# Optimization experiments

Hardware: AMD Instinct MI355X
Metric: run time of the kernel (lower is better)

## Reference

```python
import jax, jax.numpy as jnp
import numpy as np

B, S, IN_DIM, OUT_DIM = 16, 1024, 1024, 1024
NEG_SLOPE = 0.01  # torch F.leaky_relu default


def setup_inputs() -> dict:
    key = jax.random.key(0)
    ks = jax.random.split(key, 10)
    sc_in = 1.0 / np.sqrt(IN_DIM)
    sc_out = 1.0 / np.sqrt(OUT_DIM)
    return {
        "xs": jax.random.normal(ks[0], (B, S, IN_DIM), dtype=jnp.float32),
        "mask": jax.random.randint(ks[1], (B, S), 0, 2, dtype=jnp.int32),
        "Wk": jax.random.uniform(ks[2], (OUT_DIM, IN_DIM), jnp.float32, -sc_in, sc_in),
        "bk": jax.random.uniform(ks[3], (OUT_DIM,), jnp.float32, -sc_in, sc_in),
        "Wq": jax.random.uniform(ks[4], (OUT_DIM, IN_DIM), jnp.float32, -sc_in, sc_in),
        "bq": jax.random.uniform(ks[5], (OUT_DIM,), jnp.float32, -sc_in, sc_in),
        "Wv": jax.random.uniform(ks[6], (OUT_DIM, IN_DIM), jnp.float32, -sc_in, sc_in),
        "bv": jax.random.uniform(ks[7], (OUT_DIM,), jnp.float32, -sc_in, sc_in),
        "Wlin": jax.random.uniform(ks[8], (OUT_DIM, OUT_DIM), jnp.float32, -sc_out, sc_out),
        "blin": jax.random.uniform(ks[9], (OUT_DIM,), jnp.float32, -sc_out, sc_out),
    }


def reference(xs, mask, Wk, bk, Wq, bq, Wv, bv, Wlin, blin):
    # projections: torch Linear is x @ W.T + b
    K = jnp.einsum('bsi,oi->bso', xs, Wk) + bk  # [B,S,D]
    Q = jnp.einsum('bsi,oi->bso', xs, Wq) + bq  # [B,S,D]
    V = jnp.einsum('bsi,oi->bso', xs, Wv) + bv  # [B,S,D]
    # qk[b,s,e] = sum_d K[b,s,d] * Q[b,e,d]
    qk = jnp.einsum('bsd,bed->bse', K, Q) / xs.shape[-1]
    # mask.repeat(1,S).view(B,S,S) => element [b,i,j] = mask[b,j] (column/key mask)
    qk = jnp.where(mask[:, None, :].astype(bool), qk, -jnp.inf)
    a = jax.nn.softmax(qk, axis=-1)  # [B,S,S]
    # faithful to einsum('bij,bik->bik'): sum a over last axis, scale V elementwise
    attn = jnp.sum(a, axis=-1, keepdims=True) * V  # [B,S,D]
    out = jnp.einsum('bsd,od->bso', attn, Wlin) + blin
    return jnp.where(out >= 0, out, NEG_SLOPE * out)
```

## Files before the change

### kernel.cpp

```cpp
#include <hip/hip_runtime.h>
#include <hip/hip_bf16.h>
#include <stdint.h>


#define M_TOT 16384
#define KDIM  1024
#define NDIM  1024
#define NKT   16

typedef __attribute__((ext_vector_type(8))) short bf16x8;
typedef __attribute__((ext_vector_type(4))) float f32x4;
typedef __attribute__((ext_vector_type(4))) unsigned short u16x4;
typedef __attribute__((ext_vector_type(8))) unsigned short u16x8;

static __device__ __forceinline__ unsigned short f2bf(float f) {
    union { float f; unsigned int u; } v; v.f = f;
    unsigned int u = v.u;
    return (unsigned short)((u + 0x7fffu + ((u >> 16) & 1u)) >> 16);
}

static __device__ __forceinline__ u16x8 pack8(float4 a, float4 b) {
    u16x8 p = { f2bf(a.x), f2bf(a.y), f2bf(a.z), f2bf(a.w),
                f2bf(b.x), f2bf(b.y), f2bf(b.z), f2bf(b.w) };
    return p;
}

static __device__ __forceinline__ void gload16(const void* g, void* l) {
    __builtin_amdgcn_global_load_lds(
        (__attribute__((address_space(1))) void*)(g),
        (__attribute__((address_space(3))) void*)(l), 16, 0, 0);
}

static __device__ __forceinline__ int swz128(int p) {
    return p ^ (((p >> 7) & 7) << 4);
}

__global__ __launch_bounds__(256) void prep0_kernel(
    const float* __restrict__ Wv, const float* __restrict__ Wlin,
    const float* __restrict__ bv, const float* __restrict__ blin,
    unsigned short* __restrict__ Wvt, unsigned short* __restrict__ Wlb,
    float* __restrict__ bcomb) {
    __shared__ float Tl[64 * 65];
    const int bid = blockIdx.x;
    const int t = threadIdx.x;

    if (bid < 256) {
        const int dt = bid >> 4;
        const int it = bid & 15;
        const int r = t >> 2;
        const int c0 = (t & 3) * 16;
        #pragma unroll
        for (int u = 0; u < 4; ++u) {
            float4 v = *(const float4*)&Wv[((size_t)(dt * 64 + r)) * NDIM + it * 64 + c0 + 4 * u];
            Tl[r * 65 + c0 + 4 * u + 0] = v.x;
            Tl[r * 65 + c0 + 4 * u + 1] = v.y;
            Tl[r * 65 + c0 + 4 * u + 2] = v.z;
            Tl[r * 65 + c0 + 4 * u + 3] = v.w;
        }
        __syncthreads();
        const int i = t >> 2;
        const int dq = (t & 3) * 16;
        float v[16];
        #pragma unroll
        for (int u = 0; u < 16; ++u) v[u] = Tl[(dq + u) * 65 + i];
        u16x8 p0 = { f2bf(v[0]), f2bf(v[1]), f2bf(v[2]), f2bf(v[3]),
                     f2bf(v[4]), f2bf(v[5]), f2bf(v[6]), f2bf(v[7]) };
        u16x8 p1 = { f2bf(v[8]), f2bf(v[9]), f2bf(v[10]), f2bf(v[11]),
                     f2bf(v[12]), f2bf(v[13]), f2bf(v[14]), f2bf(v[15]) };
        unsigned short* dst = &Wvt[((size_t)(it * 64 + i)) * KDIM + dt * 64 + dq];
        *(u16x8*)dst = p0;
        *(u16x8*)(dst + 8) = p1;
    } else if (bid < 512) {
        const size_t idx = (((size_t)(bid - 256)) * 256 + t) * 16;
        float4 a = *(const float4*)&Wlin[idx];
        float4 b = *(const float4*)&Wlin[idx + 4];
        float4 c = *(const float4*)&Wlin[idx + 8];
        float4 d = *(const float4*)&Wlin[idx + 12];
        *(u16x8*)&Wlb[idx] = pack8(a, b);
        *(u16x8*)&Wlb[idx + 8] = pack8(c, d);
    } else {
        const int wave = t >> 6, lane = t & 63;
        const int o = (bid - 512) * 4 + wave;
        float s = 0.f;
        for (int d = lane; d < KDIM; d += 64) s += Wlin[o * KDIM + d] * bv[d];
        #pragma unroll
        for (int off = 32; off > 0; off >>= 1) s += __shfl_down(s, off, 64);
        if (lane == 0) bcomb[o] = s + blin[o];
    }
}

__global__ __launch_bounds__(256) void wcomb_kernel(
    const unsigned short* __restrict__ Wlb, const unsigned short* __restrict__ Wvt,
    unsigned short* __restrict__ Wc) {
    __shared__ unsigned short As[64 * 32];
    __shared__ unsigned short Bs[64 * 32];
    const int t = threadIdx.x;
    const int ot = blockIdx.x >> 4;
    const int it = blockIdx.x & 15;
    const int w = t >> 6, l = t & 63;
    const int wr = (w >> 1) * 32, wc = (w & 1) * 32;
    const int lr = l & 15, lk = l >> 4;

    f32x4 acc[2][2] = {};

    const unsigned short* gA = &Wlb[((size_t)(ot * 64 + (t >> 2))) * KDIM + (t & 3) * 8];
    const unsigned short* gB = &Wvt[((size_t)(it * 64 + (t >> 2))) * KDIM + (t & 3) * 8];
    unsigned short* lA = &As[w * 512];
    unsigned short* lB = &Bs[w * 512];

    for (int kt = 0; kt < KDIM / 32; ++kt) {
        gload16(gA + kt * 32, lA);
        gload16(gB + kt * 32, lB);
        __syncthreads();
        bf16x8 af[2], bfr[2];
        #pragma unroll
        for (int fi = 0; fi < 2; ++fi)
            af[fi] = *(bf16x8*)&As[(wr + fi * 16 + lr) * 32 + lk * 8];
        #pragma unroll
        for (int fj = 0; fj < 2; ++fj)
            bfr[fj] = *(bf16x8*)&Bs[(wc + fj * 16 + lr) * 32 + lk * 8];
        #pragma unroll
        for (int fi = 0; fi < 2; ++fi)
            #pragma unroll
            for (int fj = 0; fj < 2; ++fj)
                acc[fi][fj] = __builtin_amdgcn_mfma_f32_16x16x32_bf16(
                    af[fi], bfr[fj], acc[fi][fj], 0, 0, 0);
        __syncthreads();
    }
    #pragma unroll
    for (int fi = 0; fi < 2; ++fi)
        #pragma unroll
        for (int fj = 0; fj < 2; ++fj)
            #pragma unroll
            for (int r = 0; r < 4; ++r) {
                const int o = ot * 64 + wr + fi * 16 + lk * 4 + r;
                const int i = it * 64 + wc + fj * 16 + lr;
                Wc[(size_t)o * KDIM + i] = f2bf(acc[fi][fj][r]);
            }
}

__global__ __launch_bounds__(512, 2) void main_fused(
    const float* __restrict__ xs, const unsigned short* __restrict__ Wc,
    const float* __restrict__ bcomb, float* __restrict__ out) {
    extern __shared__ char lds[];
    const int tid = threadIdx.x;
    const int w = tid >> 6, l = tid & 63;
    const int wm = w >> 2, wn = w & 3;
    const int lr = l & 15, lk = l >> 4;

    const int swzb = ((blockIdx.x & 7) << 5) + (blockIdx.x >> 3);
    const int mt = swzb >> 2, nt = swzb & 3;

    int aoff[8], boff[4];
    #pragma unroll
    for (int fi = 0; fi < 8; ++fi)
        aoff[fi] = swz128((wm * 128 + fi * 16 + lr) * 128 + lk * 16);
    #pragma unroll
    for (int fj = 0; fj < 4; ++fj)
        boff[fj] = 32768 + swz128((wn * 64 + fj * 16 + lr) * 128 + lk * 16);

    const float* gA[4];
    int awr[4];
    #pragma unroll
    for (int j = 0; j < 4; ++j) {
        const int row = j * 64 + (tid >> 3);
        gA[j] = xs + ((size_t)(mt * 256 + row)) * KDIM + (tid & 7) * 8;
        awr[j] = swz128(row * 128 + (tid & 7) * 16);
    }
    const char* gB[4];
    #pragma unroll
    for (int j = 0; j < 4; ++j) {
        const int q = j * 8192 + w * 1024 + l * 16;
        const int p = swz128(q);
        gB[j] = (const char*)Wc + ((size_t)(nt * 256 + (p >> 7))) * 2048 + (p & 127);
    }
    const int bofs[4] = { 32768 + w * 1024, 32768 + 8192 + w * 1024,
                          32768 + 16384 + w * 1024, 32768 + 24576 + w * 1024 };

    f32x4 acc[8][4] = {};
    float4 avA[8];

#define STAGE_A(TT)                                                            \
    _Pragma("unroll")                                                          \
    for (int j = 0; j < 4; ++j) {                                              \
        avA[2 * j]     = *(const float4*)(gA[j] + (TT) * 64);                  \
        avA[2 * j + 1] = *(const float4*)(gA[j] + (TT) * 64 + 4);              \
    }

    STAGE_A(0);
    #pragma unroll
    for (int j = 0; j < 4; ++j)
        gload16(gB[j], lds + bofs[j]);
    *(u16x8*)(lds + awr[0]) = pack8(avA[0], avA[1]);
    *(u16x8*)(lds + awr[1]) = pack8(avA[2], avA[3]);
    *(u16x8*)(lds + awr[2]) = pack8(avA[4], avA[5]);
    *(u16x8*)(lds + awr[3]) = pack8(avA[6], avA[7]);
    asm volatile("s_waitcnt vmcnt(0)" ::: "memory");
    asm volatile("s_waitcnt lgkmcnt(0)" ::: "memory");
    __builtin_amdgcn_s_barrier();

#define MFMA16(ACCI, AF, BF)                                                   \
    _Pragma("unroll")                                                          \
    for (int fi = 0; fi < 4; ++fi)                                             \
        _Pragma("unroll")                                                      \
        for (int fj = 0; fj < 4; ++fj)                                         \
            acc[(ACCI) + fi][fj] = __builtin_amdgcn_mfma_f32_16x16x32_bf16(    \
                (AF)[fi], (BF)[fj], acc[(ACCI) + fi][fj], 0, 0, 0)

#define PH_SYNC()                                                              \
    __builtin_amdgcn_s_barrier();                                              \
    asm volatile("s_waitcnt lgkmcnt(0)" ::: "memory");                         \
    __builtin_amdgcn_sched_barrier(0)

#define ITER(T, SEN, WN)                                                       \
    do {                                                                       \
        const char* cbuf = lds + (((T) & 1) << 16);                            \
        char* nbuf = lds + ((((T) & 1) ^ 1) << 16);                            \
        if (SEN) {                                                             \
            STAGE_A((T) + 1);                                                  \
            gload16(gB[0] + ((size_t)(T) + 1) * 128, nbuf + bofs[0]);          \
            gload16(gB[1] + ((size_t)(T) + 1) * 128, nbuf + bofs[1]);          \
            gload16(gB[2] + ((size_t)(T) + 1) * 128, nbuf + bofs[2]);          \
            gload16(gB[3] + ((size_t)(T) + 1) * 128, nbuf + bofs[3]);          \
        }                                                                      \
        asm volatile("s_waitcnt vmcnt(" #WN ")" ::: "memory");                 \
        __builtin_amdgcn_s_barrier();                                          \
                                               \
        bf16x8 b0[4], a0[4];                                                   \
        _Pragma("unroll")                                                      \
        for (int fj = 0; fj < 4; ++fj)                                         \
            b0[fj] = *(const bf16x8*)(cbuf + boff[fj]);                        \
        _Pragma("unroll")                                                      \
        for (int fi = 0; fi < 4; ++fi)                                         \
            a0[fi] = *(const bf16x8*)(cbuf + aoff[fi]);                        \
        PH_SYNC();                                                             \
        __builtin_amdgcn_s_setprio(1);                                         \
        MFMA16(0, a0, b0);                                                     \
        __builtin_amdgcn_s_setprio(0);                                         \
        __builtin_amdgcn_s_barrier();                                          \
                                                       \
        bf16x8 a1[4];                                                          \
        _Pragma("unroll")                                                      \
        for (int fi = 0; fi < 4; ++fi)                                         \
            a1[fi] = *(const bf16x8*)(cbuf + aoff[4 + fi]);                    \
        PH_SYNC();                                                             \
        __builtin_amdgcn_s_setprio(1);                                         \
        MFMA16(4, a1, b0);                                                     \
        __builtin_amdgcn_s_setprio(0);                                         \
        __builtin_amdgcn_s_barrier();                                          \
                    \
        bf16x8 b1[4], a2[4];                                                   \
        _Pragma("unroll")                                                      \
        for (int fj = 0; fj < 4; ++fj)                                         \
            b1[fj] = *(const bf16x8*)(cbuf + (boff[fj] ^ 64));                 \
        _Pragma("unroll")                                                      \
        for (int fi = 0; fi < 4; ++fi)                                         \
            a2[fi] = *(const bf16x8*)(cbuf + (aoff[fi] ^ 64));                 \
        PH_SYNC();                                                             \
        __builtin_amdgcn_s_setprio(1);                                         \
        MFMA16(0, a2, b1);                                                     \
        __builtin_amdgcn_s_setprio(0);                                         \
        if (SEN) {                                                             \
            *(u16x8*)(nbuf + awr[0]) = pack8(avA[0], avA[1]);                  \
            *(u16x8*)(nbuf + awr[1]) = pack8(avA[2], avA[3]);                  \
        }                                                                      \
        __builtin_amdgcn_s_barrier();                                          \
                            \
        bf16x8 a3[4];                                                          \
        _Pragma("unroll")                                                      \
        for (int fi = 0; fi < 4; ++fi)                                         \
            a3[fi] = *(const bf16x8*)(cbuf + (aoff[4 + fi] ^ 64));             \
        PH_SYNC();                                                             \
        __builtin_amdgcn_s_setprio(1);                                         \
        MFMA16(4, a3, b1);                                                     \
        __builtin_amdgcn_s_setprio(0);                                         \
        if (SEN) {                                                             \
            *(u16x8*)(nbuf + awr[2]) = pack8(avA[4], avA[5]);                  \
            *(u16x8*)(nbuf + awr[3]) = pack8(avA[6], avA[7]);                  \
        }                                                                      \
    } while (0)

    for (int t = 0; t < NKT - 1; ++t) {
        ITER(t, 1, 12);
    }
    ITER(15, 0, 0);
#undef ITER
#undef PH_SYNC
#undef MFMA16
#undef STAGE_A

    #pragma unroll
    for (int fi = 0; fi < 8; ++fi)
        #pragma unroll
        for (int fj = 0; fj < 4; ++fj) {
            const int col = nt * 256 + wn * 64 + fj * 16 + lr;
            const float b = bcomb[col];
            #pragma unroll
            for (int r = 0; r < 4; ++r) {
                const int row = mt * 256 + wm * 128 + fi * 16 + lk * 4 + r;
                float v = acc[fi][fj][r] + b;
                out[(size_t)row * NDIM + col] = v >= 0.f ? v : 0.01f * v;
            }
        }
}

__global__ __launch_bounds__(256) void main_gemm_f32(
    const float* __restrict__ X, const unsigned short* __restrict__ Wc,
    const float* __restrict__ bcomb, float* __restrict__ out) {
    __shared__ unsigned short As[128 * 32];
    __shared__ unsigned short Bs[128 * 32];
    const int t = threadIdx.x;
    const int nt = blockIdx.x & 7;
    const int mt = blockIdx.x >> 3;
    const int w = t >> 6, l = t & 63;
    const int wr = (w >> 1) * 64, wcc = (w & 1) * 64;
    const int lr = l & 15, lk = l >> 4;

    f32x4 acc[4][4] = {};

    const int arow = t >> 3;
    const int akq = t & 7;
    const int brow = t >> 2;
    const int bc4 = t & 3;

    for (int kt = 0; kt < KDIM / 32; ++kt) {
        float4 av[4];
        #pragma unroll
        for (int j = 0; j < 4; ++j) {
            const int row = j * 32 + arow;
            av[j] = *(const float4*)&X[(mt * 128 + row) * KDIM + kt * 32 + akq * 4];
        }
        __syncthreads();
        #pragma unroll
        for (int j = 0; j < 4; ++j) {
            const int row = j * 32 + arow;
            u16x4 p = { f2bf(av[j].x), f2bf(av[j].y), f2bf(av[j].z), f2bf(av[j].w) };
            *(u16x4*)&As[row * 32 + akq * 4] = p;
        }
        #pragma unroll
        for (int j = 0; j < 2; ++j) {
            const int row = j * 64 + brow;
            const unsigned short* g = &Wc[(nt * 128 + row) * KDIM + kt * 32 + bc4 * 8];
            unsigned short* ldst = &Bs[(j * 256 + w * 64) * 8];
            gload16(g, ldst);
        }
        __syncthreads();
        bf16x8 af[4], bfr[4];
        #pragma unroll
        for (int fi = 0; fi < 4; ++fi)
            af[fi] = *(bf16x8*)&As[(wr + fi * 16 + lr) * 32 + lk * 8];
        #pragma unroll
        for (int fj = 0; fj < 4; ++fj)
            bfr[fj] = *(bf16x8*)&Bs[(wcc + fj * 16 + lr) * 32 + lk * 8];
        #pragma unroll
        for (int fi = 0; fi < 4; ++fi)
            #pragma unroll
            for (int fj = 0; fj < 4; ++fj)
                acc[fi][fj] = __builtin_amdgcn_mfma_f32_16x16x32_bf16(
                    af[fi], bfr[fj], acc[fi][fj], 0, 0, 0);
    }

    #pragma unroll
    for (int fi = 0; fi < 4; ++fi)
        #pragma unroll
        for (int fj = 0; fj < 4; ++fj) {
            const int col = nt * 128 + wcc + fj * 16 + lr;
            const float b = bcomb[col];
            #pragma unroll
            for (int r = 0; r < 4; ++r) {
                const int row = mt * 128 + wr + fi * 16 + lk * 4 + r;
                float v = acc[fi][fj][r] + b;
                out[row * NDIM + col] = v >= 0.f ? v : 0.01f * v;
            }
        }
}

extern "C" void kernel_launch(void* const* d_in, const int* in_sizes, int n_in,
                              void* d_out, int out_size, void* d_ws, size_t ws_size,
                              hipStream_t stream) {
    const float* xs   = (const float*)d_in[0];
    const float* Wv   = (const float*)d_in[6];
    const float* bv   = (const float*)d_in[7];
    const float* Wlin = (const float*)d_in[8];
    const float* blin = (const float*)d_in[9];

    unsigned short* Wc = (unsigned short*)d_ws;
    float* bcomb = (float*)((char*)d_ws + 2097152);
    float* out = (float*)d_out;

    unsigned short* Wvt = (unsigned short*)d_out;
    unsigned short* Wlb = (unsigned short*)((char*)d_out + 2097152);

    const size_t NEED = 2101248;
    hipLaunchKernelGGL(prep0_kernel, dim3(768), dim3(256), 0, stream,
                       Wv, Wlin, bv, blin, Wvt, Wlb, bcomb);
    hipLaunchKernelGGL(wcomb_kernel, dim3(256), dim3(256), 0, stream,
                       Wlb, Wvt, Wc);
    if (ws_size >= NEED) {
        (void)hipFuncSetAttribute((const void*)main_fused,
                                  hipFuncAttributeMaxDynamicSharedMemorySize,
                                  131072);
        hipLaunchKernelGGL(main_fused, dim3(256), dim3(512), 131072, stream,
                           xs, Wc, bcomb, out);
    } else {
        hipLaunchKernelGGL(main_gemm_f32, dim3((M_TOT / 128) * (NDIM / 128)),
                           dim3(256), 0, stream, xs, Wc, bcomb, out);
    }
}
```

Baseline: 79.13 us.

## Switch fused GEMM to 4-buffer ring with 32-wide K tiles and prefetch depth two

Halves the K tile from 64 to 32 elements and uses a four-slot LDS ring instead of double buffering, so global loads for A and B are issued two iterations ahead. The LDS swizzle is changed to fit the 64-byte row layout, and each iteration is reduced from four sync phases to two. The goal is to hide global-load latency better and cut barrier and waitcnt overhead per MFMA block. In exchange there are twice as many iterations, each with less work between barriers, and the new swizzle may cause more LDS bank conflicts.

```diff
diff --git a/kernel.cpp b/kernel.cpp
--- a/kernel.cpp
+++ b/kernel.cpp
@@ -6,7 +6,7 @@
 #define M_TOT 16384
 #define KDIM  1024
 #define NDIM  1024
-#define NKT   16
+#define NKT   32
 
 typedef __attribute__((ext_vector_type(8))) short bf16x8;
 typedef __attribute__((ext_vector_type(4))) float f32x4;
@@ -31,8 +31,8 @@
         (__attribute__((address_space(3))) void*)(l), 16, 0, 0);
 }
 
-static __device__ __forceinline__ int swz128(int p) {
-    return p ^ (((p >> 7) & 7) << 4);
+static __device__ __forceinline__ int swz(int p) {
+    return p ^ (((p >> 9) & 1) << 5) ^ (((p >> 8) & 1) << 4);
 }
 
 __global__ __launch_bounds__(256) void prep0_kernel(
@@ -154,48 +154,55 @@
     int aoff[8], boff[4];
     #pragma unroll
     for (int fi = 0; fi < 8; ++fi)
-        aoff[fi] = swz128((wm * 128 + fi * 16 + lr) * 128 + lk * 16);
+        aoff[fi] = swz((wm * 128 + fi * 16 + lr) * 64 + lk * 16);
     #pragma unroll
     for (int fj = 0; fj < 4; ++fj)
-        boff[fj] = 32768 + swz128((wn * 64 + fj * 16 + lr) * 128 + lk * 16);
-
-    const float* gA[4];
-    int awr[4];
-    #pragma unroll
-    for (int j = 0; j < 4; ++j) {
-        const int row = j * 64 + (tid >> 3);
-        gA[j] = xs + ((size_t)(mt * 256 + row)) * KDIM + (tid & 7) * 8;
-        awr[j] = swz128(row * 128 + (tid & 7) * 16);
-    }
-    const char* gB[4];
-    #pragma unroll
-    for (int j = 0; j < 4; ++j) {
-        const int q = j * 8192 + w * 1024 + l * 16;
-        const int p = swz128(q);
-        gB[j] = (const char*)Wc + ((size_t)(nt * 256 + (p >> 7))) * 2048 + (p & 127);
-    }
-    const int bofs[4] = { 32768 + w * 1024, 32768 + 8192 + w * 1024,
-                          32768 + 16384 + w * 1024, 32768 + 24576 + w * 1024 };
+        boff[fj] = 16384 + swz((wn * 64 + fj * 16 + lr) * 64 + lk * 16);
+
+    const float* gAq[2];
+    const char* gBq[2];
+    #pragma unroll
+    for (int c = 0; c < 2; ++c) {
+        const int q = c * 8192 + tid * 16;
+        const int p = swz(q);
+        const int row = p >> 6;
+        const int colb = p & 63;
+        gAq[c] = xs + ((size_t)(mt * 256 + row)) * KDIM + (colb >> 1);
+        gBq[c] = (const char*)Wc + ((size_t)(nt * 256 + row)) * 2048 + colb;
+    }
+    const int ldsA0 = tid * 16;
+    const int ldsA1 = 8192 + tid * 16;
+    const int ldsBw = 16384 + w * 1024;
 
     f32x4 acc[8][4] = {};
-    float4 avA[8];
-
-#define STAGE_A(TT)                                                            \
-    _Pragma("unroll")                                                          \
-    for (int j = 0; j < 4; ++j) {                                              \
-        avA[2 * j]     = *(const float4*)(gA[j] + (TT) * 64);                  \
-        avA[2 * j + 1] = *(const float4*)(gA[j] + (TT) * 64 + 4);              \
-    }
-
-    STAGE_A(0);
-    #pragma unroll
-    for (int j = 0; j < 4; ++j)
-        gload16(gB[j], lds + bofs[j]);
-    *(u16x8*)(lds + awr[0]) = pack8(avA[0], avA[1]);
-    *(u16x8*)(lds + awr[1]) = pack8(avA[2], avA[3]);
-    *(u16x8*)(lds + awr[2]) = pack8(avA[4], avA[5]);
-    *(u16x8*)(lds + awr[3]) = pack8(avA[6], avA[7]);
-    asm volatile("s_waitcnt vmcnt(0)" ::: "memory");
+    float4 avA[4];
+
+#define LOAD_A(TT)                                                             \
+    do {                                                                       \
+        avA[0] = *(const float4*)(gAq[0] + (TT) * 32);                         \
+        avA[1] = *(const float4*)(gAq[0] + (TT) * 32 + 4);                     \
+        avA[2] = *(const float4*)(gAq[1] + (TT) * 32);                         \
+        avA[3] = *(const float4*)(gAq[1] + (TT) * 32 + 4);                     \
+    } while (0)
+
+#define CVT_A(BUF)                                                             \
+    do {                                                                       \
+        *(u16x8*)((BUF) + ldsA0) = pack8(avA[0], avA[1]);                      \
+        *(u16x8*)((BUF) + ldsA1) = pack8(avA[2], avA[3]);                      \
+    } while (0)
+
+#define GLOAD_B(TT, BUF)                                                       \
+    do {                                                                       \
+        gload16(gBq[0] + (size_t)(TT) * 64, (BUF) + ldsBw);                    \
+        gload16(gBq[1] + (size_t)(TT) * 64, (BUF) + 8192 + ldsBw);             \
+    } while (0)
+
+    LOAD_A(0);
+    GLOAD_B(0, lds);
+    CVT_A(lds);
+    LOAD_A(1);
+    GLOAD_B(1, lds + 32768);
+    CVT_A(lds + 32768);
     asm volatile("s_waitcnt lgkmcnt(0)" ::: "memory");
     __builtin_amdgcn_s_barrier();
 
@@ -207,87 +214,52 @@
             acc[(ACCI) + fi][fj] = __builtin_amdgcn_mfma_f32_16x16x32_bf16(    \
                 (AF)[fi], (BF)[fj], acc[(ACCI) + fi][fj], 0, 0, 0)
 
-#define PH_SYNC()                                                              \
-    __builtin_amdgcn_s_barrier();                                              \
-    asm volatile("s_waitcnt lgkmcnt(0)" ::: "memory");                         \
-    __builtin_amdgcn_sched_barrier(0)
-
 #define ITER(T, SEN, WN)                                                       \
     do {                                                                       \
-        const char* cbuf = lds + (((T) & 1) << 16);                            \
-        char* nbuf = lds + ((((T) & 1) ^ 1) << 16);                            \
-        if (SEN) {                                                             \
-            STAGE_A((T) + 1);                                                  \
-            gload16(gB[0] + ((size_t)(T) + 1) * 128, nbuf + bofs[0]);          \
-            gload16(gB[1] + ((size_t)(T) + 1) * 128, nbuf + bofs[1]);          \
-            gload16(gB[2] + ((size_t)(T) + 1) * 128, nbuf + bofs[2]);          \
-            gload16(gB[3] + ((size_t)(T) + 1) * 128, nbuf + bofs[3]);          \
-        }                                                                      \
-        asm volatile("s_waitcnt vmcnt(" #WN ")" ::: "memory");                 \
-        __builtin_amdgcn_s_barrier();                                          \
-                                               \
-        bf16x8 b0[4], a0[4];                                                   \
+        const char* cbuf = lds + (size_t)((T) & 3) * 32768;                    \
+        char* stbuf = lds + (size_t)(((T) + 2) & 3) * 32768;                   \
+                  \
+        if (SEN) { LOAD_A((T) + 2); }                                          \
+        bf16x8 bfr[4], afr[4];                                                 \
         _Pragma("unroll")                                                      \
         for (int fj = 0; fj < 4; ++fj)                                         \
-            b0[fj] = *(const bf16x8*)(cbuf + boff[fj]);                        \
+            bfr[fj] = *(const bf16x8*)(cbuf + boff[fj]);                       \
         _Pragma("unroll")                                                      \
         for (int fi = 0; fi < 4; ++fi)                                         \
-            a0[fi] = *(const bf16x8*)(cbuf + aoff[fi]);                        \
-        PH_SYNC();                                                             \
+            afr[fi] = *(const bf16x8*)(cbuf + aoff[fi]);                       \
+        __builtin_amdgcn_s_barrier();                                          \
         __builtin_amdgcn_s_setprio(1);                                         \
-        MFMA16(0, a0, b0);                                                     \
+        MFMA16(0, afr, bfr);                                                   \
         __builtin_amdgcn_s_setprio(0);                                         \
         __builtin_amdgcn_s_barrier();                                          \
-                                                       \
-        bf16x8 a1[4];                                                          \
+                          \
+        if (SEN) { GLOAD_B((T) + 2, stbuf); }                                  \
+        bf16x8 af2[4];                                                         \
         _Pragma("unroll")                                                      \
         for (int fi = 0; fi < 4; ++fi)                                         \
-            a1[fi] = *(const bf16x8*)(cbuf + aoff[4 + fi]);                    \
-        PH_SYNC();                                                             \
+            af2[fi] = *(const bf16x8*)(cbuf + aoff[4 + fi]);                   \
+        __builtin_amdgcn_s_barrier();                                          \
         __builtin_amdgcn_s_setprio(1);                                         \
-        MFMA16(4, a1, b0);                                                     \
+        MFMA16(4, af2, bfr);                                                   \
         __builtin_amdgcn_s_setprio(0);                                         \
+            \
+        if (SEN) { CVT_A(stbuf); }                                             \
+                                                            \
+        asm volatile("s_waitcnt vmcnt(" #WN ")" ::: "memory");                 \
+        asm volatile("s_waitcnt lgkmcnt(0)" ::: "memory");                     \
         __builtin_amdgcn_s_barrier();                                          \
-                    \
-        bf16x8 b1[4], a2[4];                                                   \
-        _Pragma("unroll")                                                      \
-        for (int fj = 0; fj < 4; ++fj)                                         \
-            b1[fj] = *(const bf16x8*)(cbuf + (boff[fj] ^ 64));                 \
-        _Pragma("unroll")                                                      \
-        for (int fi = 0; fi < 4; ++fi)                                         \
-            a2[fi] = *(const bf16x8*)(cbuf + (aoff[fi] ^ 64));                 \
-        PH_SYNC();                                                             \
-        __builtin_amdgcn_s_setprio(1);                                         \
-        MFMA16(0, a2, b1);                                                     \
-        __builtin_amdgcn_s_setprio(0);                                         \
-        if (SEN) {                                                             \
-            *(u16x8*)(nbuf + awr[0]) = pack8(avA[0], avA[1]);                  \
-            *(u16x8*)(nbuf + awr[1]) = pack8(avA[2], avA[3]);                  \
-        }                                                                      \
-        __builtin_amdgcn_s_barrier();                                          \
-                            \
-        bf16x8 a3[4];                                                          \
-        _Pragma("unroll")                                                      \
-        for (int fi = 0; fi < 4; ++fi)                                         \
-            a3[fi] = *(const bf16x8*)(cbuf + (aoff[4 + fi] ^ 64));             \
-        PH_SYNC();                                                             \
-        __builtin_amdgcn_s_setprio(1);                                         \
-        MFMA16(4, a3, b1);                                                     \
-        __builtin_amdgcn_s_setprio(0);                                         \
-        if (SEN) {                                                             \
-            *(u16x8*)(nbuf + awr[2]) = pack8(avA[4], avA[5]);                  \
-            *(u16x8*)(nbuf + awr[3]) = pack8(avA[6], avA[7]);                  \
-        }                                                                      \
     } while (0)
 
-    for (int t = 0; t < NKT - 1; ++t) {
-        ITER(t, 1, 12);
-    }
-    ITER(15, 0, 0);
+    for (int t = 0; t < NKT - 2; ++t) {
+        ITER(t, 1, 2);
+    }
+    ITER(30, 0, 2);
+    ITER(31, 0, 0);
 #undef ITER
-#undef PH_SYNC
 #undef MFMA16
-#undef STAGE_A
+#undef GLOAD_B
+#undef CVT_A
+#undef LOAD_A
 
     #pragma unroll
     for (int fi = 0; fi < 8; ++fi)
```

Measured after the change: 82.21 us. +3.9%, slower.

## Pre-convert xs to bf16 in prep kernel and use direct-to-LDS loads for both operands

Applied to the files above, without the earlier changes.

Adds an xs-to-bf16 conversion pass to the weight-combining prep kernel, writing a bf16 copy of the activations into workspace. The main GEMM then loads both A and B tiles straight into LDS with async global loads, replacing the fp32 register staging, packing and LDS writes. B is prefetched two tiles ahead and A one tile ahead, with the waits and barriers rearranged to match. This removes conversion and LDS-store work from the GEMM's inner loop. In exchange, the xs array is read in fp32 once and written plus re-read in bf16, which adds extra memory traffic and a larger workspace requirement.

```diff
diff --git a/kernel.cpp b/kernel.cpp
--- a/kernel.cpp
+++ b/kernel.cpp
@@ -89,14 +89,29 @@
     }
 }
 
-__global__ __launch_bounds__(256) void wcomb_kernel(
+__global__ __launch_bounds__(256) void prep1_kernel(
     const unsigned short* __restrict__ Wlb, const unsigned short* __restrict__ Wvt,
-    unsigned short* __restrict__ Wc) {
+    const float* __restrict__ xs, unsigned short* __restrict__ Wc,
+    unsigned short* __restrict__ Xb) {
     __shared__ unsigned short As[64 * 32];
     __shared__ unsigned short Bs[64 * 32];
+    const int bid = blockIdx.x;
     const int t = threadIdx.x;
-    const int ot = blockIdx.x >> 4;
-    const int it = blockIdx.x & 15;
+
+    if (bid >= 256) {
+        const size_t base = (((size_t)(bid - 256)) * 256 + t) * 8;
+        #pragma unroll
+        for (int itr = 0; itr < 4; ++itr) {
+            const size_t idx = base + (size_t)itr * (size_t)(2048 * 256 * 8);
+            float4 a = *(const float4*)&xs[idx];
+            float4 b = *(const float4*)&xs[idx + 4];
+            *(u16x8*)&Xb[idx] = pack8(a, b);
+        }
+        return;
+    }
+
+    const int ot = bid >> 4;
+    const int it = bid & 15;
     const int w = t >> 6, l = t & 63;
     const int wr = (w >> 1) * 32, wc = (w & 1) * 32;
     const int lr = l & 15, lk = l >> 4;
@@ -139,8 +154,8 @@
             }
 }
 
-__global__ __launch_bounds__(512, 2) void main_fused(
-    const float* __restrict__ xs, const unsigned short* __restrict__ Wc,
+__global__ __launch_bounds__(512, 2) void main_8p(
+    const unsigned short* __restrict__ Xb, const unsigned short* __restrict__ Wc,
     const float* __restrict__ bcomb, float* __restrict__ out) {
     extern __shared__ char lds[];
     const int tid = threadIdx.x;
@@ -159,44 +174,39 @@
     for (int fj = 0; fj < 4; ++fj)
         boff[fj] = 32768 + swz128((wn * 64 + fj * 16 + lr) * 128 + lk * 16);
 
-    const float* gA[4];
-    int awr[4];
-    #pragma unroll
-    for (int j = 0; j < 4; ++j) {
-        const int row = j * 64 + (tid >> 3);
-        gA[j] = xs + ((size_t)(mt * 256 + row)) * KDIM + (tid & 7) * 8;
-        awr[j] = swz128(row * 128 + (tid & 7) * 16);
-    }
-    const char* gB[4];
+    const char* srcA[4];
+    const char* srcB[4];
     #pragma unroll
     for (int j = 0; j < 4; ++j) {
         const int q = j * 8192 + w * 1024 + l * 16;
         const int p = swz128(q);
-        gB[j] = (const char*)Wc + ((size_t)(nt * 256 + (p >> 7))) * 2048 + (p & 127);
-    }
-    const int bofs[4] = { 32768 + w * 1024, 32768 + 8192 + w * 1024,
-                          32768 + 16384 + w * 1024, 32768 + 24576 + w * 1024 };
+        const int r = p >> 7, c = p & 127;
+        srcA[j] = (const char*)Xb + ((size_t)(mt * 256 + r) * KDIM) * 2 + c;
+        srcB[j] = (const char*)Wc + ((size_t)(nt * 256 + r) * KDIM) * 2 + c;
+    }
+    const int ldsw = w * 1024;
 
     f32x4 acc[8][4] = {};
-    float4 avA[8];
-
-#define STAGE_A(TT)                                                            \
-    _Pragma("unroll")                                                          \
-    for (int j = 0; j < 4; ++j) {                                              \
-        avA[2 * j]     = *(const float4*)(gA[j] + (TT) * 64);                  \
-        avA[2 * j + 1] = *(const float4*)(gA[j] + (TT) * 64 + 4);              \
-    }
-
-    STAGE_A(0);
-    #pragma unroll
-    for (int j = 0; j < 4; ++j)
-        gload16(gB[j], lds + bofs[j]);
-    *(u16x8*)(lds + awr[0]) = pack8(avA[0], avA[1]);
-    *(u16x8*)(lds + awr[1]) = pack8(avA[2], avA[3]);
-    *(u16x8*)(lds + awr[2]) = pack8(avA[4], avA[5]);
-    *(u16x8*)(lds + awr[3]) = pack8(avA[6], avA[7]);
-    asm volatile("s_waitcnt vmcnt(0)" ::: "memory");
-    asm volatile("s_waitcnt lgkmcnt(0)" ::: "memory");
+
+#define GLOAD_A(T, BUF)                                                        \
+    do {                                                                       \
+        gload16(srcA[0] + (size_t)(T) * 128, (BUF) + 0 * 8192 + ldsw);         \
+        gload16(srcA[1] + (size_t)(T) * 128, (BUF) + 1 * 8192 + ldsw);         \
+        gload16(srcA[2] + (size_t)(T) * 128, (BUF) + 2 * 8192 + ldsw);         \
+        gload16(srcA[3] + (size_t)(T) * 128, (BUF) + 3 * 8192 + ldsw);         \
+    } while (0)
+#define GLOAD_B(T, BUF)                                                        \
+    do {                                                                       \
+        gload16(srcB[0] + (size_t)(T) * 128, (BUF) + 32768 + 0 * 8192 + ldsw); \
+        gload16(srcB[1] + (size_t)(T) * 128, (BUF) + 32768 + 1 * 8192 + ldsw); \
+        gload16(srcB[2] + (size_t)(T) * 128, (BUF) + 32768 + 2 * 8192 + ldsw); \
+        gload16(srcB[3] + (size_t)(T) * 128, (BUF) + 32768 + 3 * 8192 + ldsw); \
+    } while (0)
+
+    GLOAD_A(0, lds);
+    GLOAD_B(0, lds);
+    GLOAD_B(1, lds + 65536);
+    asm volatile("s_waitcnt vmcnt(4)" ::: "memory");
     __builtin_amdgcn_s_barrier();
 
 #define MFMA16(ACCI, AF, BF)                                                   \
@@ -207,25 +217,14 @@
             acc[(ACCI) + fi][fj] = __builtin_amdgcn_mfma_f32_16x16x32_bf16(    \
                 (AF)[fi], (BF)[fj], acc[(ACCI) + fi][fj], 0, 0, 0)
 
-#define PH_SYNC()                                                              \
-    __builtin_amdgcn_s_barrier();                                              \
-    asm volatile("s_waitcnt lgkmcnt(0)" ::: "memory");                         \
-    __builtin_amdgcn_sched_barrier(0)
-
-#define ITER(T, SEN, WN)                                                       \
+#define LGKM0() asm volatile("s_waitcnt lgkmcnt(0)" ::: "memory")
+
+#define KTILE(T, SA, SB, WN)                                                   \
     do {                                                                       \
         const char* cbuf = lds + (((T) & 1) << 16);                            \
         char* nbuf = lds + ((((T) & 1) ^ 1) << 16);                            \
-        if (SEN) {                                                             \
-            STAGE_A((T) + 1);                                                  \
-            gload16(gB[0] + ((size_t)(T) + 1) * 128, nbuf + bofs[0]);          \
-            gload16(gB[1] + ((size_t)(T) + 1) * 128, nbuf + bofs[1]);          \
-            gload16(gB[2] + ((size_t)(T) + 1) * 128, nbuf + bofs[2]);          \
-            gload16(gB[3] + ((size_t)(T) + 1) * 128, nbuf + bofs[3]);          \
-        }                                                                      \
-        asm volatile("s_waitcnt vmcnt(" #WN ")" ::: "memory");                 \
-        __builtin_amdgcn_s_barrier();                                          \
-                                               \
+        char* cbw = lds + (((T) & 1) << 16);                                   \
+                               \
         bf16x8 b0[4], a0[4];                                                   \
         _Pragma("unroll")                                                      \
         for (int fj = 0; fj < 4; ++fj)                                         \
@@ -233,22 +232,25 @@
         _Pragma("unroll")                                                      \
         for (int fi = 0; fi < 4; ++fi)                                         \
             a0[fi] = *(const bf16x8*)(cbuf + aoff[fi]);                        \
-        PH_SYNC();                                                             \
+        if (SA) { GLOAD_A((T) + 1, nbuf); }                                    \
+        __builtin_amdgcn_s_barrier();                                          \
+        LGKM0();                                                               \
         __builtin_amdgcn_s_setprio(1);                                         \
         MFMA16(0, a0, b0);                                                     \
         __builtin_amdgcn_s_setprio(0);                                         \
         __builtin_amdgcn_s_barrier();                                          \
-                                                       \
+                                                     \
         bf16x8 a1[4];                                                          \
         _Pragma("unroll")                                                      \
         for (int fi = 0; fi < 4; ++fi)                                         \
             a1[fi] = *(const bf16x8*)(cbuf + aoff[4 + fi]);                    \
-        PH_SYNC();                                                             \
+        __builtin_amdgcn_s_barrier();                                          \
+        LGKM0();                                                               \
         __builtin_amdgcn_s_setprio(1);                                         \
         MFMA16(4, a1, b0);                                                     \
         __builtin_amdgcn_s_setprio(0);                                         \
         __builtin_amdgcn_s_barrier();                                          \
-                    \
+                                             \
         bf16x8 b1[4], a2[4];                                                   \
         _Pragma("unroll")                                                      \
         for (int fj = 0; fj < 4; ++fj)                                         \
@@ -256,38 +258,38 @@
         _Pragma("unroll")                                                      \
         for (int fi = 0; fi < 4; ++fi)                                         \
             a2[fi] = *(const bf16x8*)(cbuf + (aoff[fi] ^ 64));                 \
-        PH_SYNC();                                                             \
+        __builtin_amdgcn_s_barrier();                                          \
+        LGKM0();                                                               \
         __builtin_amdgcn_s_setprio(1);                                         \
         MFMA16(0, a2, b1);                                                     \
         __builtin_amdgcn_s_setprio(0);                                         \
-        if (SEN) {                                                             \
-            *(u16x8*)(nbuf + awr[0]) = pack8(avA[0], avA[1]);                  \
-            *(u16x8*)(nbuf + awr[1]) = pack8(avA[2], avA[3]);                  \
-        }                                                                      \
-        __builtin_amdgcn_s_barrier();                                          \
-                            \
+        __builtin_amdgcn_s_barrier();                                          \
+           \
         bf16x8 a3[4];                                                          \
         _Pragma("unroll")                                                      \
         for (int fi = 0; fi < 4; ++fi)                                         \
             a3[fi] = *(const bf16x8*)(cbuf + (aoff[4 + fi] ^ 64));             \
-        PH_SYNC();                                                             \
+        if (SB) { GLOAD_B((T) + 2, cbw); }                                     \
+        __builtin_amdgcn_s_barrier();                                          \
+        LGKM0();                                                               \
         __builtin_amdgcn_s_setprio(1);                                         \
         MFMA16(4, a3, b1);                                                     \
         __builtin_amdgcn_s_setprio(0);                                         \
-        if (SEN) {                                                             \
-            *(u16x8*)(nbuf + awr[2]) = pack8(avA[4], avA[5]);                  \
-            *(u16x8*)(nbuf + awr[3]) = pack8(avA[6], avA[7]);                  \
-        }                                                                      \
+                            \
+        asm volatile("s_waitcnt vmcnt(" #WN ")" ::: "memory");                 \
+        __builtin_amdgcn_s_barrier();                                          \
     } while (0)
 
-    for (int t = 0; t < NKT - 1; ++t) {
-        ITER(t, 1, 12);
-    }
-    ITER(15, 0, 0);
-#undef ITER
-#undef PH_SYNC
+    for (int t = 0; t < NKT - 2; ++t) {
+        KTILE(t, 1, 1, 4);
+    }
+    KTILE(14, 1, 0, 0);
+    KTILE(15, 0, 0, 0);
+#undef KTILE
+#undef LGKM0
 #undef MFMA16
-#undef STAGE_A
+#undef GLOAD_B
+#undef GLOAD_A
 
     #pragma unroll
     for (int fi = 0; fi < 8; ++fi)
@@ -386,23 +388,26 @@
 
     unsigned short* Wc = (unsigned short*)d_ws;
     float* bcomb = (float*)((char*)d_ws + 2097152);
+    unsigned short* Xb = (unsigned short*)((char*)d_ws + 2101248);
     float* out = (float*)d_out;
 
     unsigned short* Wvt = (unsigned short*)d_out;
     unsigned short* Wlb = (unsigned short*)((char*)d_out + 2097152);
 
-    const size_t NEED = 2101248;
+    const size_t NEED = 2101248 + (size_t)M_TOT * KDIM * 2;
     hipLaunchKernelGGL(prep0_kernel, dim3(768), dim3(256), 0, stream,
                        Wv, Wlin, bv, blin, Wvt, Wlb, bcomb);
-    hipLaunchKernelGGL(wcomb_kernel, dim3(256), dim3(256), 0, stream,
-                       Wlb, Wvt, Wc);
     if (ws_size >= NEED) {
-        (void)hipFuncSetAttribute((const void*)main_fused,
+        (void)hipFuncSetAttribute((const void*)main_8p,
                                   hipFuncAttributeMaxDynamicSharedMemorySize,
                                   131072);
-        hipLaunchKernelGGL(main_fused, dim3(256), dim3(512), 131072, stream,
-                           xs, Wc, bcomb, out);
+        hipLaunchKernelGGL(prep1_kernel, dim3(256 + 2048), dim3(256), 0, stream,
+                           Wlb, Wvt, xs, Wc, Xb);
+        hipLaunchKernelGGL(main_8p, dim3(256), dim3(512), 131072, stream,
+                           Xb, Wc, bcomb, out);
     } else {
+        hipLaunchKernelGGL(prep1_kernel, dim3(256), dim3(256), 0, stream,
+                           Wlb, Wvt, xs, Wc, Xb);
         hipLaunchKernelGGL(main_gemm_f32, dim3((M_TOT / 128) * (NDIM / 128)),
                            dim3(256), 0, stream, xs, Wc, bcomb, out);
     }
```

New measurement: 74.13 us. 1.07x faster.
